# Kernel tuning notes

Hardware: AMD Instinct MI355X
Metric: run time of the kernel (lower is better)

## Reference

```python
import jax, jax.numpy as jnp
import numpy as np


def gcn_conv(x, edge_index, edge_weight, W, b):
    """PyG GCNConv: add self-loops (weight 1), symmetric normalization,
    linear transform, edge-weighted scatter-add aggregation, bias."""
    N = x.shape[0]
    src = jnp.concatenate([edge_index[0], jnp.arange(N, dtype=edge_index.dtype)])
    dst = jnp.concatenate([edge_index[1], jnp.arange(N, dtype=edge_index.dtype)])
    ew = jnp.concatenate([edge_weight, jnp.ones((N,), dtype=edge_weight.dtype)])
    # deg over destination nodes (source_to_target flow)
    deg = jax.ops.segment_sum(ew, dst, num_segments=N)
    dinv = jnp.where(deg > 0, deg ** -0.5, 0.0).astype(x.dtype)
    norm = dinv[src] * ew * dinv[dst]          # [E+N]
    xw = x @ W                                  # [N, out] linear first (cheaper)
    msgs = norm[:, None] * xw[src]              # [E+N, out]
    out = jax.ops.segment_sum(msgs, dst, num_segments=N)
    return out + b


def setup_inputs() -> dict:
    key = jax.random.key(0)
    ks = jax.random.split(key, 7)
    N, E, F_in, H, F_out = 100000, 1600000, 394, 256, 64
    x = jax.random.normal(ks[0], (N, F_in), dtype=jnp.float32)
    edge_index = jax.random.randint(ks[1], (2, E), 0, N, dtype=jnp.int32)
    edge_weight = jax.random.uniform(ks[2], (E,), dtype=jnp.float32)
    W1 = jax.random.normal(ks[3], (F_in, H), dtype=jnp.float32) * (1.0 / np.sqrt(F_in))
    b1 = jnp.zeros((H,), dtype=jnp.float32)
    W2 = jax.random.normal(ks[4], (H, F_out), dtype=jnp.float32) * (1.0 / np.sqrt(H))
    b2 = jnp.zeros((F_out,), dtype=jnp.float32)
    return {"x": x, "edge_index": edge_index, "edge_weight": edge_weight,
            "W1": W1, "b1": b1, "W2": W2, "b2": b2}


def reference(x, edge_index, edge_weight, W1, b1, W2, b2):
    h = gcn_conv(x, edge_index, edge_weight, W1, b1)
    h = jax.nn.relu(h)
    # F.dropout(training=self.training) is identity in eval mode
    out = gcn_conv(h, edge_index, edge_weight, W2, b2)
    return out
```

## Files before the change

kernel.cpp:

```cpp
#include <hip/hip_runtime.h>
#include <hip/hip_bf16.h>
#include <hip/hip_fp16.h>
#include <type_traits>


typedef _Float16 f16x8 __attribute__((ext_vector_type(8)));
typedef float f32x4 __attribute__((ext_vector_type(4)));

__device__ inline void async_copy16(const void* g, void* l) {
    __builtin_amdgcn_global_load_lds(
        (const __attribute__((address_space(1))) void*)g,
        (__attribute__((address_space(3))) void*)l, 16, 0, 0);
}


__global__ __launch_bounds__(256) void init_node(float* packed, int N) {
    int i = blockIdx.x * 256 + threadIdx.x;
    if (i < N) {
        packed[2 * i] = 1.0f;
        ((int*)packed)[2 * i + 1] = 0;
    }
}

__global__ __launch_bounds__(256) void accum_deg_hist(const int* __restrict__ dst,
                                                      const float* __restrict__ ew,
                                                      float* packed, int E) {
    int e = blockIdx.x * 256 + threadIdx.x;
    if (e < E) {
        int d = dst[e];
        atomicAdd(&packed[2 * d], ew[e]);
        atomicAdd(&((int*)packed)[2 * d + 1], 1);
    }
}

__global__ __launch_bounds__(256) void compute_dinv(const float* __restrict__ packed,
                                                    float* __restrict__ dinv, int N) {
    int i = blockIdx.x * 256 + threadIdx.x;
    if (i < N) dinv[i] = rsqrtf(packed[2 * i]);
}

#define SCAN_TILE 2048

__global__ __launch_bounds__(256) void scan1(const float* __restrict__ packed,
                                             int* __restrict__ rowptr,
                                             int* __restrict__ bsums, int N) {
    __shared__ int tmp[256];
    int t = threadIdx.x;
    int base = blockIdx.x * SCAN_TILE + t * 8;
    const int* pc = (const int*)packed;
    int v[8], s = 0;
#pragma unroll
    for (int j = 0; j < 8; ++j) { v[j] = (base + j < N) ? pc[2 * (base + j) + 1] : 0; s += v[j]; }
    tmp[t] = s;
    __syncthreads();
#pragma unroll
    for (int off = 1; off < 256; off <<= 1) {
        int u = (t >= off) ? tmp[t - off] : 0;
        __syncthreads();
        tmp[t] += u;
        __syncthreads();
    }
    int run = tmp[t] - s;
#pragma unroll
    for (int j = 0; j < 8; ++j) {
        if (base + j < N) rowptr[base + j] = run;
        run += v[j];
    }
    if (t == 255) bsums[blockIdx.x] = tmp[255];
}

__global__ __launch_bounds__(256) void scan2(int* bsums, int* rowptr, int NB, int N, int E) {
    __shared__ int tmp[256];
    int t = threadIdx.x;
    int v = (t < NB) ? bsums[t] : 0;
    tmp[t] = v;
    __syncthreads();
#pragma unroll
    for (int off = 1; off < 256; off <<= 1) {
        int u = (t >= off) ? tmp[t - off] : 0;
        __syncthreads();
        tmp[t] += u;
        __syncthreads();
    }
    if (t < NB) bsums[t] = tmp[t] - v;
    if (t == 0) rowptr[N] = E;
}

__global__ __launch_bounds__(256) void scan3(int* rowptr, int* cursor,
                                             const int* __restrict__ bsums, int N) {
    int base = blockIdx.x * SCAN_TILE + threadIdx.x * 8;
    int off = bsums[blockIdx.x];
#pragma unroll
    for (int j = 0; j < 8; ++j)
        if (base + j < N) {
            int v = rowptr[base + j] + off;
            rowptr[base + j] = v;
            cursor[base + j] = v;
        }
}

__global__ __launch_bounds__(256) void fill_csr(const int* __restrict__ src,
                                                const int* __restrict__ dst,
                                                const float* __restrict__ ew,
                                                const float* __restrict__ dinv,
                                                int* __restrict__ cursor,
                                                int2* __restrict__ cv, int E) {
    int e = blockIdx.x * 256 + threadIdx.x;
    if (e < E) {
        int d = dst[e], s = src[e];
        int pos = atomicAdd(&cursor[d], 1);
        float v = dinv[s] * ew[e] * dinv[d];
        cv[pos] = make_int2(s, __float_as_int(v));
    }
}

__global__ __launch_bounds__(256) void tohalf_w(const float* __restrict__ W,
                                                __half* __restrict__ WT,
                                                int K, int N, int Kpad) {
    int idx = blockIdx.x * 256 + threadIdx.x;
    int total = N * Kpad;
    if (idx >= total) return;
    int n = idx / Kpad, k = idx % Kpad;
    float v = (k < K) ? W[(size_t)k * N + n] : 0.0f;
    WT[idx] = __float2half(v);
}

__global__ __launch_bounds__(256) void tohalf_x(const float* __restrict__ x,
                                                __half* __restrict__ Xh,
                                                int Nn, int K, int Kpad) {
    int idx = blockIdx.x * 256 + threadIdx.x;
    int cpr = Kpad / 8;
    int total = Nn * cpr;
    if (idx >= total) return;
    int row = idx / cpr, c = idx % cpr;
    int gk = c * 8;
    const float* p = x + (size_t)row * K + gk;
    float v[8];
    if (gk + 8 <= K) {
#pragma unroll
        for (int j = 0; j < 4; ++j) {
            float2 t2 = *(const float2*)(p + j * 2);
            v[j * 2] = t2.x; v[j * 2 + 1] = t2.y;
        }
    } else {
#pragma unroll
        for (int j = 0; j < 8; ++j) v[j] = (gk + j < K) ? p[j] : 0.0f;
    }
    union { __half2 h[4]; uint4 u; } pk;
#pragma unroll
    for (int j = 0; j < 4; ++j) pk.h[j] = __floats2half2_rn(v[j * 2], v[j * 2 + 1]);
    *(uint4*)&Xh[(size_t)row * Kpad + gk] = pk.u;
}

template <int BM, int BN, int WARPS_M, int WARPS_N, int NT>
__global__ __launch_bounds__(NT) void gemm_f16(const __half* __restrict__ Ah,
                                               const __half* __restrict__ BT,
                                               __half* __restrict__ C,
                                               int M, int Kpad) {
    const int WM = BM / WARPS_M, WN = BN / WARPS_N;
    const int FM = WM / 16, FN = WN / 16;
    const int ACH = BM * 4;
    const int BCH = BN * 4;
    const int TOTCH = ACH + BCH;
    const int CH = TOTCH / NT;
    static_assert(CH == 3, "vmcnt(3) hardcoded below");
    __shared__ __align__(16) __half lds[2][TOTCH * 8];

    int tid = threadIdx.x;
    int lane = tid & 63;
    int w = tid >> 6;
    int wr = w / WARPS_N, wc = w % WARPS_N;
    int bm = blockIdx.x * BM;
    int lrow = lane & 15;
    int lslot = lane >> 4;

    const __half* srcp[CH];
#pragma unroll
    for (int i = 0; i < CH; ++i) {
        int ch = tid + i * NT;
        if (ch < ACH) {
            int c = ch, row = c >> 2;
            int grow = bm + row;
            if (grow >= M) grow = M - 1;
            srcp[i] = Ah + (size_t)grow * Kpad + (size_t)(((c & 3) ^ ((row >> 1) & 3)) * 8);
        } else {
            int c = ch - ACH, row = c >> 2;
            srcp[i] = BT + (size_t)row * Kpad + (size_t)(((c & 3) ^ ((row >> 1) & 3)) * 8);
        }
    }

    f32x4 acc[FM][FN];
#pragma unroll
    for (int m = 0; m < FM; ++m)
#pragma unroll
        for (int n = 0; n < FN; ++n) acc[m][n] = (f32x4){0.f, 0.f, 0.f, 0.f};

    auto stage = [&](int buf) {
#pragma unroll
        for (int i = 0; i < CH; ++i) {
            async_copy16(srcp[i], &lds[buf][(size_t)((tid & ~63) + i * NT) * 8]);
            srcp[i] += 32;
        }
    };

    auto compute = [&](int buf) {
        f16x8 af[FM], bf[FN];
#pragma unroll
        for (int m = 0; m < FM; ++m) {
            int row = wr * WM + m * 16 + lrow;
            int p = lslot ^ ((row >> 1) & 3);
            af[m] = *(const f16x8*)&lds[buf][(size_t)(row * 4 + p) * 8];
        }
#pragma unroll
        for (int n = 0; n < FN; ++n) {
            int row = wc * WN + n * 16 + lrow;
            int p = lslot ^ ((row >> 1) & 3);
            bf[n] = *(const f16x8*)&lds[buf][(size_t)(ACH + row * 4 + p) * 8];
        }
#pragma unroll
        for (int m = 0; m < FM; ++m)
#pragma unroll
            for (int n = 0; n < FN; ++n)
                acc[m][n] = __builtin_amdgcn_mfma_f32_16x16x32_f16(af[m], bf[n], acc[m][n], 0, 0, 0);
    };

    const int nsteps = Kpad / 32;
    stage(0);
    for (int s = 0; s < nsteps; ++s) {
        if (s + 1 < nsteps) {
            stage((s + 1) & 1);
            asm volatile("s_waitcnt vmcnt(3)" ::: "memory");
        } else {
            asm volatile("s_waitcnt vmcnt(0)" ::: "memory");
        }
        __builtin_amdgcn_s_barrier();
        compute(s & 1);
        __builtin_amdgcn_s_barrier();
    }

#pragma unroll
    for (int m = 0; m < FM; ++m) {
        int rb = bm + wr * WM + m * 16 + (lane >> 4) * 4;
#pragma unroll
        for (int n = 0; n < FN; ++n) {
            int cb = wc * WN + n * 16 + (lane & 15);
#pragma unroll
            for (int i = 0; i < 4; ++i) {
                int r = rb + i;
                if (r < M) C[(size_t)r * BN + cb] = __float2half(acc[m][n][i]);
            }
        }
    }
}

template <int F, int LPN, int RELU, typename OutT>
__global__ __launch_bounds__(256) void gatherh(const int* __restrict__ rowptr,
                                               const int2* __restrict__ cv,
                                               const __half* __restrict__ xw,
                                               const float* __restrict__ dinv,
                                               const float* __restrict__ bias,
                                               OutT* __restrict__ out, int N) {
    const int NPB = 256 / LPN;
    int d = blockIdx.x * NPB + threadIdx.x / LPN;
    if (d >= N) return;
    int lane = threadIdx.x % LPN;

    float di = dinv[d];
    float w = di * di;
    uint2 raw = *(const uint2*)(xw + (size_t)d * F + lane * 4);
    float2 u0 = __half22float2(*(__half2*)&raw.x);
    float2 u1 = __half22float2(*(__half2*)&raw.y);
    float a0 = w * u0.x, a1 = w * u0.y, a2 = w * u1.x, a3 = w * u1.y;
    float b0 = 0.f, b1 = 0.f, b2 = 0.f, b3 = 0.f;

    int p = rowptr[d], p1 = rowptr[d + 1];
    for (; p + 4 <= p1; p += 4) {
        int2 e0 = cv[p], e1 = cv[p + 1], e2 = cv[p + 2], e3 = cv[p + 3];
        uint2 r0 = *(const uint2*)(xw + (size_t)e0.x * F + lane * 4);
        uint2 r1 = *(const uint2*)(xw + (size_t)e1.x * F + lane * 4);
        uint2 r2 = *(const uint2*)(xw + (size_t)e2.x * F + lane * 4);
        uint2 r3 = *(const uint2*)(xw + (size_t)e3.x * F + lane * 4);
        float w0 = __int_as_float(e0.y), w1 = __int_as_float(e1.y);
        float w2 = __int_as_float(e2.y), w3 = __int_as_float(e3.y);
        {
            float2 v0 = __half22float2(*(__half2*)&r0.x);
            float2 v1 = __half22float2(*(__half2*)&r0.y);
            a0 = fmaf(w0, v0.x, a0); a1 = fmaf(w0, v0.y, a1);
            a2 = fmaf(w0, v1.x, a2); a3 = fmaf(w0, v1.y, a3);
        }
        {
            float2 v0 = __half22float2(*(__half2*)&r1.x);
            float2 v1 = __half22float2(*(__half2*)&r1.y);
            b0 = fmaf(w1, v0.x, b0); b1 = fmaf(w1, v0.y, b1);
            b2 = fmaf(w1, v1.x, b2); b3 = fmaf(w1, v1.y, b3);
        }
        {
            float2 v0 = __half22float2(*(__half2*)&r2.x);
            float2 v1 = __half22float2(*(__half2*)&r2.y);
            a0 = fmaf(w2, v0.x, a0); a1 = fmaf(w2, v0.y, a1);
            a2 = fmaf(w2, v1.x, a2); a3 = fmaf(w2, v1.y, a3);
        }
        {
            float2 v0 = __half22float2(*(__half2*)&r3.x);
            float2 v1 = __half22float2(*(__half2*)&r3.y);
            b0 = fmaf(w3, v0.x, b0); b1 = fmaf(w3, v0.y, b1);
            b2 = fmaf(w3, v1.x, b2); b3 = fmaf(w3, v1.y, b3);
        }
    }
    for (; p < p1; ++p) {
        int2 e = cv[p];
        float wv = __int_as_float(e.y);
        uint2 rv = *(const uint2*)(xw + (size_t)e.x * F + lane * 4);
        float2 v0 = __half22float2(*(__half2*)&rv.x);
        float2 v1 = __half22float2(*(__half2*)&rv.y);
        a0 = fmaf(wv, v0.x, a0); a1 = fmaf(wv, v0.y, a1);
        a2 = fmaf(wv, v1.x, a2); a3 = fmaf(wv, v1.y, a3);
    }
    a0 += b0; a1 += b1; a2 += b2; a3 += b3;

    float4 bb = *(const float4*)&bias[lane * 4];
    a0 += bb.x; a1 += bb.y; a2 += bb.z; a3 += bb.w;
    if (RELU) {
        a0 = fmaxf(a0, 0.f); a1 = fmaxf(a1, 0.f);
        a2 = fmaxf(a2, 0.f); a3 = fmaxf(a3, 0.f);
    }
    if constexpr (std::is_same_v<OutT, float>) {
        *(float4*)&out[(size_t)d * F + lane * 4] = make_float4(a0, a1, a2, a3);
    } else {
        __half2 h0 = __floats2half2_rn(a0, a1);
        __half2 h1 = __floats2half2_rn(a2, a3);
        uint2 packed;
        packed.x = *(uint*)&h0;
        packed.y = *(uint*)&h1;
        *(uint2*)&out[(size_t)d * F + lane * 4] = packed;
    }
}

extern "C" void kernel_launch(void* const* d_in, const int* in_sizes, int n_in,
                              void* d_out, int out_size, void* d_ws, size_t ws_size,
                              hipStream_t stream) {
    const float* x  = (const float*)d_in[0];
    const int*   ei = (const int*)d_in[1];
    const float* ew = (const float*)d_in[2];
    const float* W1 = (const float*)d_in[3];
    const float* b1 = (const float*)d_in[4];
    const float* W2 = (const float*)d_in[5];
    const float* b2 = (const float*)d_in[6];
    float* out = (float*)d_out;

    const int H    = in_sizes[4];
    const int Fout = in_sizes[6];
    const int Fin  = in_sizes[3] / H;
    const int N    = in_sizes[0] / Fin;
    const int E    = in_sizes[2];

    const int Kpad1 = (Fin + 31) / 32 * 32;
    const int Kpad2 = (H + 31) / 32 * 32;

    const int* src = ei;
    const int* dst = ei + E;

    float* ws     = (float*)d_ws;
    float* packed = ws;
    float* dinv   = packed + 2 * (size_t)N;
    int*   rowptr = (int*)(dinv + N);
    int*   cursor = rowptr + N + 4;
    int*   bsums  = cursor + N + 4;
    int2*  cv     = (int2*)(bsums + 256);
    __half* bufA  = (__half*)(cv + E);
    __half* bufB  = bufA + (size_t)N * H;
    __half* xh    = bufB + (size_t)N * H;
    __half* wt1   = xh + (size_t)N * Kpad1;
    __half* wt2   = wt1 + (size_t)H * Kpad1;

    const int NB = (N + SCAN_TILE - 1) / SCAN_TILE;

    init_node<<<(N + 255) / 256, 256, 0, stream>>>(packed, N);
    accum_deg_hist<<<(E + 255) / 256, 256, 0, stream>>>(dst, ew, packed, E);
    compute_dinv<<<(N + 255) / 256, 256, 0, stream>>>(packed, dinv, N);

    scan1<<<NB, 256, 0, stream>>>(packed, rowptr, bsums, N);
    scan2<<<1, 256, 0, stream>>>(bsums, rowptr, NB, N, E);
    scan3<<<NB, 256, 0, stream>>>(rowptr, cursor, bsums, N);
    fill_csr<<<(E + 255) / 256, 256, 0, stream>>>(src, dst, ew, dinv, cursor, cv, E);

    tohalf_w<<<(H * Kpad1 + 255) / 256, 256, 0, stream>>>(W1, wt1, Fin, H, Kpad1);
    tohalf_w<<<(Fout * Kpad2 + 255) / 256, 256, 0, stream>>>(W2, wt2, H, Fout, Kpad2);
    tohalf_x<<<((size_t)N * (Kpad1 / 8) + 255) / 256, 256, 0, stream>>>(x, xh, N, Fin, Kpad1);

    gemm_f16<128, 256, 2, 4, 512><<<(N + 127) / 128, 512, 0, stream>>>(xh, wt1, bufA, N, Kpad1);

    gatherh<256, 64, 1, __half><<<(N + 3) / 4, 256, 0, stream>>>(
        rowptr, cv, bufA, dinv, b1, bufB, N);

    gemm_f16<128, 64, 2, 2, 256><<<(N + 127) / 128, 256, 0, stream>>>(bufB, wt2, bufA, N, Kpad2);

    gatherh<64, 16, 0, float><<<(N + 15) / 16, 256, 0, stream>>>(
        rowptr, cv, bufA, dinv, b2, out, N);
}
```

Before: 553.5 us.

## Pack degree and count into one 64-bit atomic, fuse dinv, stage GEMM stores via LDS

```diff
diff --git a/kernel.cpp b/kernel.cpp
--- a/kernel.cpp
+++ b/kernel.cpp
@@ -7,6 +7,8 @@
 typedef _Float16 f16x8 __attribute__((ext_vector_type(8)));
 typedef float f32x4 __attribute__((ext_vector_type(4)));
 
+#define DEG_MASK ((1ull << 42) - 1)
+
 __device__ inline void async_copy16(const void* g, void* l) {
     __builtin_amdgcn_global_load_lds(
         (const __attribute__((address_space(1))) void*)g,
@@ -14,43 +16,43 @@
 }
 
 
-__global__ __launch_bounds__(256) void init_node(float* packed, int N) {
+__global__ __launch_bounds__(256) void init_node(unsigned long long* packed, int N) {
     int i = blockIdx.x * 256 + threadIdx.x;
-    if (i < N) {
-        packed[2 * i] = 1.0f;
-        ((int*)packed)[2 * i + 1] = 0;
-    }
+    if (i < N) packed[i] = 0ull;
 }
 
 __global__ __launch_bounds__(256) void accum_deg_hist(const int* __restrict__ dst,
                                                       const float* __restrict__ ew,
-                                                      float* packed, int E) {
+                                                      unsigned long long* packed, int E) {
     int e = blockIdx.x * 256 + threadIdx.x;
     if (e < E) {
         int d = dst[e];
-        atomicAdd(&packed[2 * d], ew[e]);
-        atomicAdd(&((int*)packed)[2 * d + 1], 1);
-    }
-}
-
-__global__ __launch_bounds__(256) void compute_dinv(const float* __restrict__ packed,
-                                                    float* __restrict__ dinv, int N) {
-    int i = blockIdx.x * 256 + threadIdx.x;
-    if (i < N) dinv[i] = rsqrtf(packed[2 * i]);
+        unsigned long long add =
+            (1ull << 42) + (unsigned long long)(ew[e] * 4294967296.0f);
+        atomicAdd(&packed[d], add);
+    }
 }
 
 #define SCAN_TILE 2048
 
-__global__ __launch_bounds__(256) void scan1(const float* __restrict__ packed,
+__global__ __launch_bounds__(256) void scan1(const unsigned long long* __restrict__ packed,
                                              int* __restrict__ rowptr,
+                                             float* __restrict__ dinv,
                                              int* __restrict__ bsums, int N) {
     __shared__ int tmp[256];
     int t = threadIdx.x;
     int base = blockIdx.x * SCAN_TILE + t * 8;
-    const int* pc = (const int*)packed;
     int v[8], s = 0;
 #pragma unroll
-    for (int j = 0; j < 8; ++j) { v[j] = (base + j < N) ? pc[2 * (base + j) + 1] : 0; s += v[j]; }
+    for (int j = 0; j < 8; ++j) {
+        int idx = base + j;
+        if (idx < N) {
+            unsigned long long pv = packed[idx];
+            v[j] = (int)(pv >> 42);
+            dinv[idx] = rsqrtf(1.0f + (float)(pv & DEG_MASK) * (1.0f / 4294967296.0f));
+        } else v[j] = 0;
+        s += v[j];
+    }
     tmp[t] = s;
     __syncthreads();
 #pragma unroll
@@ -238,16 +240,29 @@
         __builtin_amdgcn_s_barrier();
     }
 
-#pragma unroll
-    for (int m = 0; m < FM; ++m) {
-        int rb = bm + wr * WM + m * 16 + (lane >> 4) * 4;
-#pragma unroll
-        for (int n = 0; n < FN; ++n) {
-            int cb = wc * WN + n * 16 + (lane & 15);
-#pragma unroll
-            for (int i = 0; i < 4; ++i) {
-                int r = rb + i;
-                if (r < M) C[(size_t)r * BN + cb] = __float2half(acc[m][n][i]);
+    __syncthreads();
+    {
+        const int LW = WN + 8;
+        __half* tile = (__half*)lds + (size_t)w * 16 * LW;
+        const int CPR = WN / 8;
+        const int CHT = (16 * CPR) / 64;
+#pragma unroll
+        for (int m = 0; m < FM; ++m) {
+            int rb = bm + wr * WM + m * 16;
+#pragma unroll
+            for (int n = 0; n < FN; ++n)
+#pragma unroll
+                for (int i = 0; i < 4; ++i)
+                    tile[((lane >> 4) * 4 + i) * LW + n * 16 + (lane & 15)] =
+                        __float2half(acc[m][n][i]);
+#pragma unroll
+            for (int c = 0; c < CHT; ++c) {
+                int ch = lane + c * 64;
+                int r = ch / CPR, cc = ch % CPR;
+                uint4 v = *(uint4*)&tile[r * LW + cc * 8];
+                int grow = rb + r;
+                if (grow < M)
+                    *(uint4*)&C[(size_t)grow * BN + wc * WN + cc * 8] = v;
             }
         }
     }
@@ -360,9 +375,8 @@
     const int* src = ei;
     const int* dst = ei + E;
 
-    float* ws     = (float*)d_ws;
-    float* packed = ws;
-    float* dinv   = packed + 2 * (size_t)N;
+    unsigned long long* packed = (unsigned long long*)d_ws;
+    float* dinv   = (float*)(packed + N);
     int*   rowptr = (int*)(dinv + N);
     int*   cursor = rowptr + N + 4;
     int*   bsums  = cursor + N + 4;
@@ -377,9 +391,8 @@
 
     init_node<<<(N + 255) / 256, 256, 0, stream>>>(packed, N);
     accum_deg_hist<<<(E + 255) / 256, 256, 0, stream>>>(dst, ew, packed, E);
-    compute_dinv<<<(N + 255) / 256, 256, 0, stream>>>(packed, dinv, N);
-
-    scan1<<<NB, 256, 0, stream>>>(packed, rowptr, bsums, N);
+
+    scan1<<<NB, 256, 0, stream>>>(packed, rowptr, dinv, bsums, N);
     scan2<<<1, 256, 0, stream>>>(bsums, rowptr, NB, N, E);
     scan3<<<NB, 256, 0, stream>>>(rowptr, cursor, bsums, N);
     fill_csr<<<(E + 255) / 256, 256, 0, stream>>>(src, dst, ew, dinv, cursor, cv, E);
```

New measurement: 476.3 us. -14.0%, faster.
